# Kernel optimization log

Measured on AMD Instinct MI355X. Metric: run time of the kernel, lower is better.

## Reference

```python
import jax, jax.numpy as jnp
import numpy as np


def setup_inputs() -> dict:
    key = jax.random.key(0)
    k1, k2 = jax.random.split(key)
    B, TOTAL_BITS, H, W = 16, 64, 128, 128
    C_OUT, N_BITS = 64, 4
    # binary bit-plane input, values in {0, 1}
    x = (jax.random.uniform(k1, (B, TOTAL_BITS, H, W)) < 0.5).astype(jnp.float32)
    # random bit-selection map: which input bit feeds each (out_channel, bit_pos)
    rp_map = jax.random.randint(k2, (C_OUT, N_BITS), 0, TOTAL_BITS)
    return {"x": x, "rp_map": rp_map}


def reference(x, rp_map):
    # bit_select_mode path of RPLayer.forward:
    #   gather n_bits_per_out random bits per output channel, then
    #   bit-pack with power-of-two weights (MAC-free projection).
    B, TB, H, W = x.shape
    C, nb = rp_map.shape
    # [B, TB, H, W] -> [B*H*W, TB]
    x_flat = x.transpose(0, 2, 3, 1).reshape(B * H * W, TB)
    # gather: [B*H*W, C, nb]  (fancy-index along bit axis, no expand needed)
    gathered = x_flat[:, rp_map]
    # power-of-two pack weights [1, 2, 4, 8, ...]
    pack_w = 2.0 ** jnp.arange(nb, dtype=x.dtype)
    packed = jnp.einsum('ncb,b->nc', gathered, pack_w)  # [B*H*W, C]
    # [B, H, W, C] -> [B, C, H, W]
    return packed.reshape(B, H, W, C).transpose(0, 3, 1, 2)
```

## Files before the change

kernel.cpp:

```cpp
#include <hip/hip_runtime.h>
#include <cstdint>
#include <cstddef>

constexpr int Bn = 16;
constexpr int TBn = 64;
constexpr int Hn = 128;
constexpr int Wn = 128;
constexpr int Cn = 64;
constexpr int HW = Hn * Wn;
constexpr int TOTAL_PIX = Bn * HW;
constexpr int PIX_PER_BLOCK = 128;
constexpr int BLOCKS = TOTAL_PIX / PIX_PER_BLOCK;
constexpr int MROW_DW = 10;

typedef const __attribute__((address_space(1))) void g_void;
typedef __attribute__((address_space(3))) void l_void;

__global__ __launch_bounds__(256) void rp_pack_glds(
    const float* __restrict__ x,
    const int* __restrict__ rp,
    float* __restrict__ out)
{
    __shared__ float s_x[TBn][PIX_PER_BLOCK];
    __shared__ int4 s_rp[Cn];
    __shared__ uint32_t m32[32 * MROW_DW];

    if (threadIdx.x < Cn) {
        s_rp[threadIdx.x] = reinterpret_cast<const int4*>(rp)[threadIdx.x];
    }

    const int b = blockIdx.x >> 7;
    const int pix0 = (blockIdx.x & 127) << 7;
    const int lane = threadIdx.x & 63;
    const int wv = threadIdx.x >> 6;

    {
        const float* gbase = x + (size_t)b * TBn * HW
                               + (size_t)(lane >> 5) * HW
                               + pix0 + (lane & 31) * 4;
        #pragma unroll
        for (int j = 0; j < 8; ++j) {
            const int pp = wv * 16 + j * 2;
            const float* gsrc = gbase + (size_t)pp * HW;
            __builtin_amdgcn_global_load_lds((g_void*)gsrc, (l_void*)&s_x[pp][0],
                                             16, 0, 0);
        }
    }
    __syncthreads();

    const int g = threadIdx.x & 31;
    const int o = threadIdx.x >> 5;

    uint32_t p0 = 0, p1 = 0, p2 = 0, p3 = 0;
    #pragma unroll
    for (int i = 0; i < 8; ++i) {
        const float4 v = *reinterpret_cast<const float4*>(&s_x[o * 8 + i][g * 4]);
        p0 |= ((__float_as_uint(v.x) >> 23) & 1u) << i;
        p1 |= ((__float_as_uint(v.y) >> 23) & 1u) << i;
        p2 |= ((__float_as_uint(v.z) >> 23) & 1u) << i;
        p3 |= ((__float_as_uint(v.w) >> 23) & 1u) << i;
    }
    m32[g * MROW_DW + o] = p0 | (p1 << 8) | (p2 << 16) | (p3 << 24);

    __syncthreads();

    uint32_t r[8];
    #pragma unroll
    for (int i = 0; i < 8; ++i) {
        r[i] = m32[g * MROW_DW + i];
    }
    uint64_t m0 = 0, m1 = 0, m2 = 0, m3 = 0;
    #pragma unroll
    for (int i = 0; i < 8; ++i) {
        m0 |= (uint64_t)((r[i]      ) & 0xffu) << (i * 8);
        m1 |= (uint64_t)((r[i] >>  8) & 0xffu) << (i * 8);
        m2 |= (uint64_t)((r[i] >> 16) & 0xffu) << (i * 8);
        m3 |= (uint64_t)((r[i] >> 24) & 0xffu) << (i * 8);
    }

    const int c0 = o * 8;
    float* ob = out + (size_t)b * Cn * HW + (size_t)c0 * HW + pix0 + g * 4;

    #pragma unroll
    for (int ci = 0; ci < 8; ++ci) {
        const int4 rr = s_rp[c0 + ci];
        const unsigned i0 = (unsigned)rr.x;
        const unsigned i1 = (unsigned)rr.y;
        const unsigned i2 = (unsigned)rr.z;
        const unsigned i3 = (unsigned)rr.w;

        float4 oo;
        oo.x = (float)((unsigned)((m0 >> i0) & 1ull)
                     | ((unsigned)((m0 >> i1) & 1ull) << 1)
                     | ((unsigned)((m0 >> i2) & 1ull) << 2)
                     | ((unsigned)((m0 >> i3) & 1ull) << 3));
        oo.y = (float)((unsigned)((m1 >> i0) & 1ull)
                     | ((unsigned)((m1 >> i1) & 1ull) << 1)
                     | ((unsigned)((m1 >> i2) & 1ull) << 2)
                     | ((unsigned)((m1 >> i3) & 1ull) << 3));
        oo.z = (float)((unsigned)((m2 >> i0) & 1ull)
                     | ((unsigned)((m2 >> i1) & 1ull) << 1)
                     | ((unsigned)((m2 >> i2) & 1ull) << 2)
                     | ((unsigned)((m2 >> i3) & 1ull) << 3));
        oo.w = (float)((unsigned)((m3 >> i0) & 1ull)
                     | ((unsigned)((m3 >> i1) & 1ull) << 1)
                     | ((unsigned)((m3 >> i2) & 1ull) << 2)
                     | ((unsigned)((m3 >> i3) & 1ull) << 3));

        *reinterpret_cast<float4*>(ob + (size_t)ci * HW) = oo;
    }
}

extern "C" void kernel_launch(void* const* d_in, const int* in_sizes, int n_in,
                              void* d_out, int out_size, void* d_ws, size_t ws_size,
                              hipStream_t stream) {
    const float* x = (const float*)d_in[0];
    const int* rp = (const int*)d_in[1];
    float* out = (float*)d_out;

    constexpr int BLOCK = 256;
    rp_pack_glds<<<BLOCKS, BLOCK, 0, stream>>>(x, rp, out);
}
```

Measured before the change: 27.01 us.

## Process two pixel tiles per block with double-buffered async LDS loads

Each block now handles 256 pixels as two 128-pixel tiles. It issues the global-to-LDS loads for both tiles up front, then uses partial vmcnt waits so work on the first tile overlaps the loads of the second. The aim is to hide load latency and amortise per-block setup, at the cost of half as many blocks and double the LDS per block, which may reduce occupancy. The kernel is already close to memory-bandwidth bound, so there is limited headroom.

```diff
diff --git a/kernel.cpp b/kernel.cpp
--- a/kernel.cpp
+++ b/kernel.cpp
@@ -4,110 +4,123 @@
 
 constexpr int Bn = 16;
 constexpr int TBn = 64;
-constexpr int Hn = 128;
-constexpr int Wn = 128;
 constexpr int Cn = 64;
-constexpr int HW = Hn * Wn;
+constexpr int HW = 128 * 128;
 constexpr int TOTAL_PIX = Bn * HW;
-constexpr int PIX_PER_BLOCK = 128;
+constexpr int PIX_PER_TILE = 128;
+constexpr int PIX_PER_BLOCK = 256;
 constexpr int BLOCKS = TOTAL_PIX / PIX_PER_BLOCK;
 constexpr int MROW_DW = 10;
 
 typedef const __attribute__((address_space(1))) void g_void;
 typedef __attribute__((address_space(3))) void l_void;
 
-__global__ __launch_bounds__(256) void rp_pack_glds(
+__global__ __launch_bounds__(256) void rp_pack_pipe(
     const float* __restrict__ x,
     const int* __restrict__ rp,
     float* __restrict__ out)
 {
-    __shared__ float s_x[TBn][PIX_PER_BLOCK];
+    __shared__ float s_x[2][TBn][PIX_PER_TILE];
     __shared__ int4 s_rp[Cn];
-    __shared__ uint32_t m32[32 * MROW_DW];
+    __shared__ uint32_t m32[2][32 * MROW_DW];
 
     if (threadIdx.x < Cn) {
         s_rp[threadIdx.x] = reinterpret_cast<const int4*>(rp)[threadIdx.x];
     }
 
-    const int b = blockIdx.x >> 7;
-    const int pix0 = (blockIdx.x & 127) << 7;
+    const int b = blockIdx.x >> 6;
+    const int pix0 = (blockIdx.x & 63) << 8;
     const int lane = threadIdx.x & 63;
     const int wv = threadIdx.x >> 6;
-
-    {
-        const float* gbase = x + (size_t)b * TBn * HW
-                               + (size_t)(lane >> 5) * HW
-                               + pix0 + (lane & 31) * 4;
-        #pragma unroll
-        for (int j = 0; j < 8; ++j) {
-            const int pp = wv * 16 + j * 2;
-            const float* gsrc = gbase + (size_t)pp * HW;
-            __builtin_amdgcn_global_load_lds((g_void*)gsrc, (l_void*)&s_x[pp][0],
-                                             16, 0, 0);
-        }
-    }
-    __syncthreads();
-
     const int g = threadIdx.x & 31;
     const int o = threadIdx.x >> 5;
 
-    uint32_t p0 = 0, p1 = 0, p2 = 0, p3 = 0;
+    const float* gb = x + (size_t)b * TBn * HW + (size_t)(lane >> 5) * HW
+                        + pix0 + (lane & 31) * 4;
+
     #pragma unroll
-    for (int i = 0; i < 8; ++i) {
-        const float4 v = *reinterpret_cast<const float4*>(&s_x[o * 8 + i][g * 4]);
-        p0 |= ((__float_as_uint(v.x) >> 23) & 1u) << i;
-        p1 |= ((__float_as_uint(v.y) >> 23) & 1u) << i;
-        p2 |= ((__float_as_uint(v.z) >> 23) & 1u) << i;
-        p3 |= ((__float_as_uint(v.w) >> 23) & 1u) << i;
+    for (int j = 0; j < 8; ++j) {
+        const int pp = wv * 16 + j * 2;
+        __builtin_amdgcn_global_load_lds((g_void*)(gb + (size_t)pp * HW),
+                                         (l_void*)&s_x[0][pp][0], 16, 0, 0);
     }
-    m32[g * MROW_DW + o] = p0 | (p1 << 8) | (p2 << 16) | (p3 << 24);
-
-    __syncthreads();
-
-    uint32_t r[8];
     #pragma unroll
-    for (int i = 0; i < 8; ++i) {
-        r[i] = m32[g * MROW_DW + i];
-    }
-    uint64_t m0 = 0, m1 = 0, m2 = 0, m3 = 0;
-    #pragma unroll
-    for (int i = 0; i < 8; ++i) {
-        m0 |= (uint64_t)((r[i]      ) & 0xffu) << (i * 8);
-        m1 |= (uint64_t)((r[i] >>  8) & 0xffu) << (i * 8);
-        m2 |= (uint64_t)((r[i] >> 16) & 0xffu) << (i * 8);
-        m3 |= (uint64_t)((r[i] >> 24) & 0xffu) << (i * 8);
+    for (int j = 0; j < 8; ++j) {
+        const int pp = wv * 16 + j * 2;
+        __builtin_amdgcn_global_load_lds((g_void*)(gb + (size_t)pp * HW + PIX_PER_TILE),
+                                         (l_void*)&s_x[1][pp][0], 16, 0, 0);
     }
 
-    const int c0 = o * 8;
-    float* ob = out + (size_t)b * Cn * HW + (size_t)c0 * HW + pix0 + g * 4;
+    asm volatile("s_waitcnt vmcnt(8) lgkmcnt(0)\n\ts_barrier" ::: "memory");
+    __builtin_amdgcn_sched_barrier(0);
 
     #pragma unroll
-    for (int ci = 0; ci < 8; ++ci) {
-        const int4 rr = s_rp[c0 + ci];
-        const unsigned i0 = (unsigned)rr.x;
-        const unsigned i1 = (unsigned)rr.y;
-        const unsigned i2 = (unsigned)rr.z;
-        const unsigned i3 = (unsigned)rr.w;
+    for (int t = 0; t < 2; ++t) {
+        uint32_t p0 = 0, p1 = 0, p2 = 0, p3 = 0;
+        #pragma unroll
+        for (int i = 0; i < 8; ++i) {
+            const float4 v = *reinterpret_cast<const float4*>(&s_x[t][o * 8 + i][g * 4]);
+            p0 |= ((__float_as_uint(v.x) >> 23) & 1u) << i;
+            p1 |= ((__float_as_uint(v.y) >> 23) & 1u) << i;
+            p2 |= ((__float_as_uint(v.z) >> 23) & 1u) << i;
+            p3 |= ((__float_as_uint(v.w) >> 23) & 1u) << i;
+        }
+        m32[t][g * MROW_DW + o] = p0 | (p1 << 8) | (p2 << 16) | (p3 << 24);
 
-        float4 oo;
-        oo.x = (float)((unsigned)((m0 >> i0) & 1ull)
-                     | ((unsigned)((m0 >> i1) & 1ull) << 1)
-                     | ((unsigned)((m0 >> i2) & 1ull) << 2)
-                     | ((unsigned)((m0 >> i3) & 1ull) << 3));
-        oo.y = (float)((unsigned)((m1 >> i0) & 1ull)
-                     | ((unsigned)((m1 >> i1) & 1ull) << 1)
-                     | ((unsigned)((m1 >> i2) & 1ull) << 2)
-                     | ((unsigned)((m1 >> i3) & 1ull) << 3));
-        oo.z = (float)((unsigned)((m2 >> i0) & 1ull)
-                     | ((unsigned)((m2 >> i1) & 1ull) << 1)
-                     | ((unsigned)((m2 >> i2) & 1ull) << 2)
-                     | ((unsigned)((m2 >> i3) & 1ull) << 3));
-        oo.w = (float)((unsigned)((m3 >> i0) & 1ull)
-                     | ((unsigned)((m3 >> i1) & 1ull) << 1)
-                     | ((unsigned)((m3 >> i2) & 1ull) << 2)
-                     | ((unsigned)((m3 >> i3) & 1ull) << 3));
+        asm volatile("s_waitcnt lgkmcnt(0)\n\ts_barrier" ::: "memory");
+        __builtin_amdgcn_sched_barrier(0);
 
-        *reinterpret_cast<float4*>(ob + (size_t)ci * HW) = oo;
+        uint32_t r[8];
+        #pragma unroll
+        for (int i = 0; i < 8; ++i) {
+            r[i] = m32[t][g * MROW_DW + i];
+        }
+        uint64_t m0 = 0, m1 = 0, m2 = 0, m3 = 0;
+        #pragma unroll
+        for (int i = 0; i < 8; ++i) {
+            m0 |= (uint64_t)((r[i]      ) & 0xffu) << (i * 8);
+            m1 |= (uint64_t)((r[i] >>  8) & 0xffu) << (i * 8);
+            m2 |= (uint64_t)((r[i] >> 16) & 0xffu) << (i * 8);
+            m3 |= (uint64_t)((r[i] >> 24) & 0xffu) << (i * 8);
+        }
+
+        const int c0 = o * 8;
+        float* ob = out + (size_t)b * Cn * HW + (size_t)c0 * HW
+                        + pix0 + t * PIX_PER_TILE + g * 4;
+
+        #pragma unroll
+        for (int ci = 0; ci < 8; ++ci) {
+            const int4 rr = s_rp[c0 + ci];
+            const unsigned i0 = (unsigned)rr.x;
+            const unsigned i1 = (unsigned)rr.y;
+            const unsigned i2 = (unsigned)rr.z;
+            const unsigned i3 = (unsigned)rr.w;
+
+            float4 oo;
+            oo.x = (float)((unsigned)((m0 >> i0) & 1ull)
+                         | ((unsigned)((m0 >> i1) & 1ull) << 1)
+                         | ((unsigned)((m0 >> i2) & 1ull) << 2)
+                         | ((unsigned)((m0 >> i3) & 1ull) << 3));
+            oo.y = (float)((unsigned)((m1 >> i0) & 1ull)
+                         | ((unsigned)((m1 >> i1) & 1ull) << 1)
+                         | ((unsigned)((m1 >> i2) & 1ull) << 2)
+                         | ((unsigned)((m1 >> i3) & 1ull) << 3));
+            oo.z = (float)((unsigned)((m2 >> i0) & 1ull)
+                         | ((unsigned)((m2 >> i1) & 1ull) << 1)
+                         | ((unsigned)((m2 >> i2) & 1ull) << 2)
+                         | ((unsigned)((m2 >> i3) & 1ull) << 3));
+            oo.w = (float)((unsigned)((m3 >> i0) & 1ull)
+                         | ((unsigned)((m3 >> i1) & 1ull) << 1)
+                         | ((unsigned)((m3 >> i2) & 1ull) << 2)
+                         | ((unsigned)((m3 >> i3) & 1ull) << 3));
+
+            *reinterpret_cast<float4*>(ob + (size_t)ci * HW) = oo;
+        }
+
+        if (t == 0) {
+            asm volatile("s_waitcnt vmcnt(8) lgkmcnt(0)\n\ts_barrier" ::: "memory");
+            __builtin_amdgcn_sched_barrier(0);
+        }
     }
 }
 
@@ -119,5 +132,5 @@
     float* out = (float*)d_out;
 
     constexpr int BLOCK = 256;
-    rp_pack_glds<<<BLOCKS, BLOCK, 0, stream>>>(x, rp, out);
+    rp_pack_pipe<<<BLOCKS, BLOCK, 0, stream>>>(x, rp, out);
 }
```

Measured after the change: 29.42 us. 1.09x slower.
